# Kernel tuning notes

Hardware: AMD Instinct MI355X
Metric: run time of the kernel (lower is better)

Reference implementation:

```python
import jax, jax.numpy as jnp
import numpy as np
from jax import lax

# ---- hyperparameters from opt ----
CONV_SIZE = 5          # box-blur kernel size
SQRT_FRAGS = 8         # h/sqrt_frags = patch size (non-overlapping unfold)
TH1_INIT = 0.5         # initial threshold (carried across fragments, as in torch)
PATCH_MEAN = 0.1       # target fraction of on-pixels per fragment
MORPH = 5              # morphology (max/min pool) window, stride 1, pad MORPH//2
TOL = 0.02
STEP = 0.0005

H = W = 4096


def setup_inputs() -> dict:
    key = jax.random.key(0)
    x = jax.random.uniform(key, (1, 1, H, W), dtype=jnp.float32)  # image in [0,1]
    blur_k = jnp.full((1, 1, CONV_SIZE, CONV_SIZE), 1.0 / CONV_SIZE ** 2,
                      dtype=jnp.float32)  # box filter, matches torch.full(...)
    return {"x": x, "blur_k": blur_k}


def _threshold_patches(patches):
    """Sequential per-fragment threshold bisection, th carried across fragments
    exactly like the torch loop mutating self.th1."""
    def frac(patch, t):  # mean of where(patch > t, 1, 0)
        return jnp.mean((patch > t).astype(jnp.float32))

    def frag_step(th, patch):
        # while mean(threshed) < target + 0.02: th -= 0.0005
        th = lax.while_loop(lambda t: frac(patch, t) < PATCH_MEAN + TOL,
                            lambda t: t - STEP, th)
        # while mean(threshed) > target - 0.02: th += 0.0005
        th = lax.while_loop(lambda t: frac(patch, t) > PATCH_MEAN - TOL,
                            lambda t: t + STEP, th)
        return th, (patch > th).astype(jnp.float32)

    _, threshed = lax.scan(frag_step, jnp.float32(TH1_INIT), patches)
    return threshed  # [SF^2, k, k]


def _morph_pool(x, is_max):
    pad = MORPH // 2
    op = x if is_max else -x
    r = lax.reduce_window(op, -jnp.inf, lax.max,
                          (1, 1, MORPH, MORPH), (1, 1, 1, 1),
                          [(0, 0), (0, 0), (pad, pad), (pad, pad)])
    return r if is_max else -r


def reference(x, blur_k):
    N, c, h, w = x.shape  # N = c = 1
    k = h // SQRT_FRAGS
    # box blur, padding='same'
    conved = lax.conv_general_dilated(x.reshape(-1, 1, h, w), blur_k,
                                      (1, 1), "SAME").reshape(N, c, h, w)
    # F.unfold with kernel=stride=k -> non-overlapping patches, row-major order
    patches = (conved.reshape(SQRT_FRAGS, k, SQRT_FRAGS, k)
               .transpose(0, 2, 1, 3)
               .reshape(SQRT_FRAGS ** 2, k, k))
    threshed = lax.stop_gradient(_threshold_patches(patches))
    # F.fold: inverse of the unfold above
    folded = (threshed.reshape(SQRT_FRAGS, SQRT_FRAGS, k, k)
              .transpose(0, 2, 1, 3)
              .reshape(N, c, h, w))
    # morphological close: max-pool then min-pool (min_pool = -maxpool(-x))
    out = _morph_pool(_morph_pool(folded, True), False)
    return out
```

## Files before the change

### kernel.cpp

```cpp
#include <hip/hip_runtime.h>
#include <stdint.h>

#define HH 4096
#define WW 4096
#define NPIX (HH * WW)
#define NBINS 8192
#define NFRAG 64
#define FRAG_PIX (512 * 512)
#define WPR 64
#define NWORDS (HH * WPR)
#define CAP 4096

#define RANK_HI 230686u
#define RANK_LO 241172u

typedef unsigned long long u64;

__device__ __forceinline__ int frag_of(int py, int px) {
  return ((py >> 9) << 3) + (px >> 9);
}

__device__ __forceinline__ int bin_of(float v) {
  int b = (int)(v * 8192.0f);
  if (b < 0) b = 0;
  if (b > NBINS - 1) b = NBINS - 1;
  return b;
}

__device__ __forceinline__ u64 spread4(u64 x) {
  x &= 0xFFFFull;
  x = (x | (x << 24)) & 0x000000FF000000FFull;
  x = (x | (x << 12)) & 0x000F000F000F000Full;
  x = (x | (x << 6))  & 0x0303030303030303ull;
  x = (x | (x << 3))  & 0x1111111111111111ull;
  return x;
}

__device__ __forceinline__ float blur_tree(const float rowbuf[5][8], int e) {
  const float K = (float)(1.0 / 25.0);
  float p[25];
#pragma unroll
  for (int i = 0; i < 25; ++i) {
    p[i] = __fmul_rn(rowbuf[i / 5][e + (i % 5)], K);
  }
  float r0 = __fadd_rn(__fadd_rn(p[0], p[8]),  p[16]);
  float r1 = __fadd_rn(__fadd_rn(p[1], p[9]),  p[17]);
  float r2 = __fadd_rn(__fadd_rn(p[2], p[10]), p[18]);
  float r3 = __fadd_rn(__fadd_rn(p[3], p[11]), p[19]);
  float r4 = __fadd_rn(__fadd_rn(p[4], p[12]), p[20]);
  float r5 = __fadd_rn(__fadd_rn(p[5], p[13]), p[21]);
  float r6 = __fadd_rn(__fadd_rn(p[6], p[14]), p[22]);
  float r7 = __fadd_rn(__fadd_rn(p[7], p[15]), p[23]);
  float res = __fadd_rn(
      __fadd_rn(__fadd_rn(r0, r1), __fadd_rn(r2, r3)),
      __fadd_rn(__fadd_rn(r4, r5), __fadd_rn(r6, r7)));
  return __fadd_rn(res, p[24]);
}

__global__ void __launch_bounds__(512)
blur_hist_kernel(const float* __restrict__ x,
                 float* __restrict__ out,
                 uint32_t* __restrict__ hist) {
  __shared__ uint32_t lh[NBINS];
  int tid = threadIdx.x;
  for (int i = tid; i < NBINS; i += 512) lh[i] = 0;
  __syncthreads();
  int f = blockIdx.x >> 4;
  int s = blockIdx.x & 15;
  int row0 = (f >> 3) * 512 + s * 32;
  int col0 = (f & 7) * 512;
  for (int it = tid; it < 8 * 128; it += 512) {
    int pr = it >> 7;
    int c4 = it & 127;
    int py = row0 + pr * 4;
    int px = col0 + c4 * 4;
    float rb[8][8];
    bool interior = (px >= 2) && (px + 5 < WW);
#pragma unroll
    for (int r = 0; r < 8; ++r) {
      int yy = py - 2 + r;
      if ((unsigned)yy >= (unsigned)HH) {
#pragma unroll
        for (int j = 0; j < 8; ++j) rb[r][j] = 0.0f;
      } else if (interior) {
        const float* rp = x + (size_t)yy * WW + px;
        float2 L = *(const float2*)(rp - 2);
        float4 M = *(const float4*)(rp);
        float2 R = *(const float2*)(rp + 4);
        rb[r][0] = L.x; rb[r][1] = L.y;
        rb[r][2] = M.x; rb[r][3] = M.y;
        rb[r][4] = M.z; rb[r][5] = M.w;
        rb[r][6] = R.x; rb[r][7] = R.y;
      } else {
#pragma unroll
        for (int j = 0; j < 8; ++j) {
          int xx = px - 2 + j;
          rb[r][j] = ((unsigned)xx < (unsigned)WW) ? x[(size_t)yy * WW + xx] : 0.0f;
        }
      }
    }
#pragma unroll
    for (int orow = 0; orow < 4; ++orow) {
      float4 res;
      res.x = blur_tree(rb + orow, 0);
      res.y = blur_tree(rb + orow, 1);
      res.z = blur_tree(rb + orow, 2);
      res.w = blur_tree(rb + orow, 3);
      *(float4*)(out + (size_t)(py + orow) * WW + px) = res;
      atomicAdd(&lh[bin_of(res.x)], 1u);
      atomicAdd(&lh[bin_of(res.y)], 1u);
      atomicAdd(&lh[bin_of(res.z)], 1u);
      atomicAdd(&lh[bin_of(res.w)], 1u);
    }
  }
  __syncthreads();
  uint32_t* hf = hist + f * NBINS;
  for (int i = tid; i < NBINS; i += 512) {
    uint32_t c = lh[i];
    if (c) atomicAdd(&hf[i], c);
  }
}

__global__ void findcrit_kernel(const uint32_t* __restrict__ hist,
                                int4* __restrict__ bins4) {
  __shared__ uint32_t segsum[256];
  __shared__ uint32_t segoff[256];
  __shared__ int4 result;
  int f = blockIdx.x;
  int tid = threadIdx.x;
  const uint32_t* hf = hist + f * NBINS;
  int base = tid * 32;
  uint32_t h32[32];
  uint32_t s = 0;
  for (int i = 0; i < 32; ++i) { h32[i] = hf[base + i]; s += h32[i]; }
  segsum[tid] = s;
  __syncthreads();
  if (tid == 0) {
    uint32_t a = 0;
    for (int i = 0; i < 256; ++i) { segoff[i] = a; a += segsum[i]; }
  }
  __syncthreads();
  uint32_t st = segoff[tid];
  uint32_t en = st + segsum[tid];
  if (st <= RANK_HI && RANK_HI < en) {
    uint32_t a = st;
    for (int i = 0; i < 32; ++i) {
      uint32_t nx = a + h32[i];
      if (RANK_HI < nx) { result.x = base + i; result.z = (int)(RANK_HI - a); break; }
      a = nx;
    }
  }
  if (st <= RANK_LO && RANK_LO < en) {
    uint32_t a = st;
    for (int i = 0; i < 32; ++i) {
      uint32_t nx = a + h32[i];
      if (RANK_LO < nx) { result.y = base + i; result.w = (int)(RANK_LO - a); break; }
      a = nx;
    }
  }
  __syncthreads();
  if (tid == 0) bins4[f] = result;
}

__global__ void __launch_bounds__(256)
gather_kernel(const float* __restrict__ blur,
              const int4* __restrict__ bins4,
              float* __restrict__ band,
              uint32_t* __restrict__ bandcnt) {
  const int T = NPIX / 16;
  int t = blockIdx.x * blockDim.x + threadIdx.x;
  float4 v[4];
#pragma unroll
  for (int k = 0; k < 4; ++k) {
    v[k] = *(const float4*)(blur + (size_t)(t + k * T) * 4);
  }
#pragma unroll
  for (int k = 0; k < 4; ++k) {
    int p0 = (t + k * T) * 4;
    int f = frag_of(p0 >> 12, p0 & (WW - 1));
    int4 info = bins4[f];
    float vv[4] = {v[k].x, v[k].y, v[k].z, v[k].w};
#pragma unroll
    for (int e = 0; e < 4; ++e) {
      int b = bin_of(vv[e]);
      if (b == info.x || b == info.y) {
        uint32_t pos = atomicAdd(&bandcnt[f], 1u);
        if (pos < CAP) band[(size_t)f * CAP + pos] = vv[e];
      }
    }
  }
}

__global__ void select_kernel(const float* __restrict__ band,
                              const uint32_t* __restrict__ bandcnt,
                              const int4* __restrict__ bins4,
                              float2* __restrict__ vhl) {
  __shared__ float wv[CAP];
  __shared__ float res[2];
  int f = blockIdx.x;
  int tid = threadIdx.x;
  int n = (int)bandcnt[f];
  if (n > CAP) n = CAP;
  for (int i = tid; i < n; i += 256) wv[i] = band[(size_t)f * CAP + i];
  __syncthreads();
  int4 info = bins4[f];
#pragma unroll
  for (int sel = 0; sel < 2; ++sel) {
    int tb = sel ? info.y : info.x;
    int k  = sel ? info.w : info.z;
    for (int i = tid; i < n; i += 256) {
      float w = wv[i];
      if (bin_of(w) != tb) continue;
      int less = 0, leq = 0;
      for (int j = 0; j < n; ++j) {
        float u = wv[j];
        if (bin_of(u) == tb) {
          less += (u < w) ? 1 : 0;
          leq  += (u <= w) ? 1 : 0;
        }
      }
      if (less <= k && k < leq) res[sel] = w;
    }
  }
  __syncthreads();
  if (tid == 0) vhl[f] = make_float2(res[0], res[1]);
}

__global__ void walk_kernel(const float2* __restrict__ vhl, float* __restrict__ th_out) {
  int lane = threadIdx.x;
  float2 mine = vhl[lane];
  float th = 0.5f;
  for (int f = 0; f < NFRAG; ++f) {
    float VH = __shfl(mine.x, f);
    float VL = __shfl(mine.y, f);
    while (th >= VH) {
#pragma unroll
      for (int i = 0; i < 16; ++i) {
        float t2 = __fadd_rn(th, -0.0005f);
        th = (th >= VH) ? t2 : th;
      }
    }
    while (th < VL) {
#pragma unroll
      for (int i = 0; i < 16; ++i) {
        float t2 = __fadd_rn(th, 0.0005f);
        th = (th < VL) ? t2 : th;
      }
    }
    if (lane == 0) th_out[f] = th;
  }
}

__global__ void __launch_bounds__(256)
mask_pack_kernel(const float* __restrict__ blur,
                 const float* __restrict__ th,
                 u64* __restrict__ pk) {
  const int T = NPIX / 16;
  int t = blockIdx.x * blockDim.x + threadIdx.x;
  float4 v[4];
#pragma unroll
  for (int k = 0; k < 4; ++k) {
    v[k] = *(const float4*)(blur + (size_t)(t + k * T) * 4);
  }
  int lane = threadIdx.x & 63;
#pragma unroll
  for (int k = 0; k < 4; ++k) {
    int g = t + k * T;
    int p0 = g * 4;
    float tf = th[frag_of(p0 >> 12, p0 & (WW - 1))];
    u64 b0 = __ballot(v[k].x > tf);
    u64 b1 = __ballot(v[k].y > tf);
    u64 b2 = __ballot(v[k].z > tf);
    u64 b3 = __ballot(v[k].w > tf);
    if ((lane & 15) == 0) {
      int sh = lane;
      u64 w = spread4(b0 >> sh) | (spread4(b1 >> sh) << 1)
            | (spread4(b2 >> sh) << 2) | (spread4(b3 >> sh) << 3);
      int base_word = ((g - lane) * 4) >> 6;
      pk[base_word + (lane >> 4)] = w;
    }
  }
}

__global__ void dilate_kernel(const u64* __restrict__ in, u64* __restrict__ out) {
  __shared__ u64 hm[68][16];
  int bx = blockIdx.x & 3;
  int by = blockIdx.x >> 2;
  int r0 = by * 64, c0 = bx * 16;
  int tid = threadIdx.x;
  for (int it = tid; it < 68 * 16; it += 256) {
    int rr = it >> 4;
    int cc = it & 15;
    int gy = r0 - 2 + rr;
    int gx = c0 + cc;
    u64 m = 0, l = 0, r = 0;
    if ((unsigned)gy < (unsigned)HH) {
      m = in[gy * WPR + gx];
      l = (gx > 0) ? in[gy * WPR + gx - 1] : 0ull;
      r = (gx < WPR - 1) ? in[gy * WPR + gx + 1] : 0ull;
    }
    hm[rr][cc] = m | (m << 1) | (m << 2) | (m >> 1) | (m >> 2)
                   | (l >> 62) | (l >> 63) | (r << 62) | (r << 63);
  }
  __syncthreads();
  for (int it = tid; it < 64 * 16; it += 256) {
    int rr = it >> 4;
    int cc = it & 15;
    u64 v = hm[rr][cc] | hm[rr + 1][cc] | hm[rr + 2][cc] | hm[rr + 3][cc] | hm[rr + 4][cc];
    out[(r0 + rr) * WPR + c0 + cc] = v;
  }
}

__global__ void erode_unpack_kernel(const u64* __restrict__ in, float* __restrict__ out) {
  __shared__ u64 hm[68][16];
  __shared__ u64 d2[64][16];
  int bx = blockIdx.x & 3;
  int by = blockIdx.x >> 2;
  int r0 = by * 64, c0 = bx * 16;
  int tid = threadIdx.x;
  for (int it = tid; it < 68 * 16; it += 256) {
    int rr = it >> 4;
    int cc = it & 15;
    int gy = r0 - 2 + rr;
    int gx = c0 + cc;
    u64 m = 0, l = 0, r = 0;
    if ((unsigned)gy < (unsigned)HH) {
      m = ~in[gy * WPR + gx];
      l = (gx > 0) ? ~in[gy * WPR + gx - 1] : 0ull;
      r = (gx < WPR - 1) ? ~in[gy * WPR + gx + 1] : 0ull;
    }
    hm[rr][cc] = m | (m << 1) | (m << 2) | (m >> 1) | (m >> 2)
                   | (l >> 62) | (l >> 63) | (r << 62) | (r << 63);
  }
  __syncthreads();
  for (int it = tid; it < 64 * 16; it += 256) {
    int rr = it >> 4;
    int cc = it & 15;
    d2[rr][cc] = hm[rr][cc] | hm[rr + 1][cc] | hm[rr + 2][cc] | hm[rr + 3][cc] | hm[rr + 4][cc];
  }
  __syncthreads();
  int colbase = c0 * 64;
  for (int it = tid; it < 64 * 256; it += 256) {
    int rr = it >> 8;
    int px0 = (it & 255) * 4;
    u64 w = d2[rr][px0 >> 6];
    int sh = px0 & 63;
    float4 o;
    o.x = (float)(1 - (int)((w >> (sh + 0)) & 1ull));
    o.y = (float)(1 - (int)((w >> (sh + 1)) & 1ull));
    o.z = (float)(1 - (int)((w >> (sh + 2)) & 1ull));
    o.w = (float)(1 - (int)((w >> (sh + 3)) & 1ull));
    *(float4*)(out + (size_t)(r0 + rr) * WW + colbase + px0) = o;
  }
}

extern "C" void kernel_launch(void* const* d_in, const int* in_sizes, int n_in,
                              void* d_out, int out_size, void* d_ws, size_t ws_size,
                              hipStream_t stream) {
  const float* x = (const float*)d_in[0];
  if (n_in > 1 && in_sizes[0] != NPIX) x = (const float*)d_in[1];
  float* out = (float*)d_out;
  char* ws = (char*)d_ws;

  const size_t OFF_HIST = 0;
  const size_t OFF_BCNT = 2097152;
  const size_t OFF_TH   = 2097408;
  const size_t OFF_PKA  = 2097664;
  const size_t OFF_PKB  = 4194816;
  const size_t OFF_BINS = 6291968;
  const size_t OFF_VHL  = 6292992;
  const size_t OFF_BAND = 6293504;
  const size_t OFF_BLUR = 8388608;
  const size_t WS_NEED  = OFF_BLUR + (size_t)NPIX * sizeof(float);
  uint32_t* hist    = (uint32_t*)(ws + OFF_HIST);
  uint32_t* bandcnt = (uint32_t*)(ws + OFF_BCNT);
  float*    th      = (float*)(ws + OFF_TH);
  u64*      PKA     = (u64*)(ws + OFF_PKA);
  u64*      PKB     = (u64*)(ws + OFF_PKB);
  int4*     bins4   = (int4*)(ws + OFF_BINS);
  float2*   vhl     = (float2*)(ws + OFF_VHL);
  float*    band    = (float*)(ws + OFF_BAND);

  float* blurred = (ws_size >= WS_NEED) ? (float*)(ws + OFF_BLUR) : out;

  const int TPB = 256;
  const int NB16 = NPIX / 16 / TPB;

  hipMemsetAsync(hist, 0, (size_t)NFRAG * NBINS * sizeof(uint32_t) + NFRAG * sizeof(uint32_t), stream);
  blur_hist_kernel<<<1024, 512, 0, stream>>>(x, blurred, hist);
  findcrit_kernel<<<NFRAG, TPB, 0, stream>>>(hist, bins4);
  gather_kernel<<<NB16, TPB, 0, stream>>>(blurred, bins4, band, bandcnt);
  select_kernel<<<NFRAG, TPB, 0, stream>>>(band, bandcnt, bins4, vhl);
  walk_kernel<<<1, 64, 0, stream>>>(vhl, th);
  mask_pack_kernel<<<NB16, TPB, 0, stream>>>(blurred, th, PKA);
  dilate_kernel<<<256, TPB, 0, stream>>>(PKA, PKB);
  erode_unpack_kernel<<<256, TPB, 0, stream>>>(PKB, out);
}
```

Before: 315.4 us.

## Aggregate gather band hits in shared memory and stagger histogram flush

The gather kernel is reorganized so each block covers a 32-row slice of a single fragment. Matching values are collected into a shared-memory buffer with LDS atomics, and the block then reserves global slots with one atomic before copying them out. This removes the many contended global atomics on the per-fragment counter. Separately, the histogram flush in blur_hist starts each block at a rotated bin offset, spreading global atomics across addresses. The risks are that the order of values in the band changes (select is order-independent) and that there are fewer threads per block of work.

```diff
diff --git a/kernel.cpp b/kernel.cpp
--- a/kernel.cpp
+++ b/kernel.cpp
@@ -10,6 +10,7 @@
 #define WPR 64
 #define NWORDS (HH * WPR)
 #define CAP 4096
+#define LCAP 2048
 
 #define RANK_HI 230686u
 #define RANK_LO 241172u
@@ -115,7 +116,9 @@
   }
   __syncthreads();
   uint32_t* hf = hist + f * NBINS;
-  for (int i = tid; i < NBINS; i += 512) {
+  int start = ((s << 9) + tid) & (NBINS - 1);
+  for (int ii = 0; ii < NBINS; ii += 512) {
+    int i = (start + ii) & (NBINS - 1);
     uint32_t c = lh[i];
     if (c) atomicAdd(&hf[i], c);
   }
@@ -167,27 +170,42 @@
               const int4* __restrict__ bins4,
               float* __restrict__ band,
               uint32_t* __restrict__ bandcnt) {
-  const int T = NPIX / 16;
-  int t = blockIdx.x * blockDim.x + threadIdx.x;
-  float4 v[4];
-#pragma unroll
-  for (int k = 0; k < 4; ++k) {
-    v[k] = *(const float4*)(blur + (size_t)(t + k * T) * 4);
-  }
-#pragma unroll
-  for (int k = 0; k < 4; ++k) {
-    int p0 = (t + k * T) * 4;
-    int f = frag_of(p0 >> 12, p0 & (WW - 1));
-    int4 info = bins4[f];
-    float vv[4] = {v[k].x, v[k].y, v[k].z, v[k].w};
+  __shared__ float lval[LCAP];
+  __shared__ uint32_t lcnt;
+  __shared__ uint32_t gbase;
+  int f = blockIdx.x >> 4;
+  int s = blockIdx.x & 15;
+  int tid = threadIdx.x;
+  if (tid == 0) lcnt = 0;
+  __syncthreads();
+  int row0 = (f >> 3) * 512 + s * 32;
+  int col0 = (f & 7) * 512;
+  int4 info = bins4[f];
+  for (int it = tid; it < 32 * 128; it += 256) {
+    int rr = it >> 7, c4 = it & 127;
+    float4 v = *(const float4*)(blur + (size_t)(row0 + rr) * WW + col0 + c4 * 4);
+    float vv[4] = {v.x, v.y, v.z, v.w};
 #pragma unroll
     for (int e = 0; e < 4; ++e) {
       int b = bin_of(vv[e]);
       if (b == info.x || b == info.y) {
-        uint32_t pos = atomicAdd(&bandcnt[f], 1u);
-        if (pos < CAP) band[(size_t)f * CAP + pos] = vv[e];
+        uint32_t p = atomicAdd(&lcnt, 1u);
+        if (p < LCAP) lval[p] = vv[e];
+        else {
+          uint32_t pos = atomicAdd(&bandcnt[f], 1u);
+          if (pos < CAP) band[(size_t)f * CAP + pos] = vv[e];
+        }
       }
     }
+  }
+  __syncthreads();
+  uint32_t n = lcnt < LCAP ? lcnt : LCAP;
+  if (tid == 0) gbase = atomicAdd(&bandcnt[f], n);
+  __syncthreads();
+  uint32_t base = gbase;
+  for (uint32_t i = tid; i < n; i += 256) {
+    uint32_t pos = base + i;
+    if (pos < CAP) band[(size_t)f * CAP + pos] = lval[i];
   }
 }
 
@@ -389,7 +407,7 @@
   hipMemsetAsync(hist, 0, (size_t)NFRAG * NBINS * sizeof(uint32_t) + NFRAG * sizeof(uint32_t), stream);
   blur_hist_kernel<<<1024, 512, 0, stream>>>(x, blurred, hist);
   findcrit_kernel<<<NFRAG, TPB, 0, stream>>>(hist, bins4);
-  gather_kernel<<<NB16, TPB, 0, stream>>>(blurred, bins4, band, bandcnt);
+  gather_kernel<<<1024, TPB, 0, stream>>>(blurred, bins4, band, bandcnt);
   select_kernel<<<NFRAG, TPB, 0, stream>>>(band, bandcnt, bins4, vhl);
   walk_kernel<<<1, 64, 0, stream>>>(vhl, th);
   mask_pack_kernel<<<NB16, TPB, 0, stream>>>(blurred, th, PKA);
```

New measurement: 260.2 us. 17.5% less time.
